# Kernel optimization log

Hardware: AMD Instinct MI355X
Metric: run time of the kernel (lower is better)

The kernel has to match this reference:

```python
import jax, jax.numpy as jnp
import numpy as np

B, XL, QL, VL, D = 8, 128, 16, 256, 256


def setup_inputs() -> dict:
    key = jax.random.key(0)
    ks = jax.random.split(key, 10)
    q = jax.random.normal(ks[0], (B, XL, QL, D), dtype=jnp.float32)
    k = jax.random.normal(ks[1], (B, XL, VL, D), dtype=jnp.float32)
    v = jax.random.normal(ks[2], (B, XL, VL, D), dtype=jnp.float32)
    # mask==True means position is masked out (filled with -10 before softmax)
    mask = jax.random.bernoulli(ks[3], 0.3, (B, XL, VL))
    s = 1.0 / np.sqrt(D)
    qw_w = jax.random.uniform(ks[4], (D, D), jnp.float32, -s, s)
    qw_b = jax.random.uniform(ks[5], (D,), jnp.float32, -s, s)
    kw_w = jax.random.uniform(ks[6], (D, D), jnp.float32, -s, s)
    kw_b = jax.random.uniform(ks[7], (D,), jnp.float32, -s, s)
    vw_w = jax.random.uniform(ks[8], (D, D), jnp.float32, -s, s)
    vw_b = jax.random.uniform(ks[9], (D,), jnp.float32, -s, s)
    return {"q": q, "k": k, "v": v, "mask": mask,
            "qw_w": qw_w, "qw_b": qw_b, "kw_w": kw_w, "kw_b": kw_b,
            "vw_w": vw_w, "vw_b": vw_b}


def reference(q, k, v, mask, qw_w, qw_b, kw_w, kw_b, vw_w, vw_b):
    # Linear projections (torch Linear: x @ W.T + b)
    qp = q @ qw_w.T + qw_b          # [b, x_l, q_l, d]
    kp = k @ kw_w.T + kw_b          # [b, x_l, v_l, d]
    vp = v @ vw_w.T + vw_b          # [b, x_l, v_l, d]
    # QK^T then max-pool over the q_l axis -> one score per value token
    scores = jnp.einsum('bxqd,bxvd->bxqv', qp, kp)   # [b, x_l, q_l, v_l]
    ta = jnp.max(scores, axis=-2)                    # [b, x_l, v_l]
    # L2-normalize over v_l (computed BEFORE masking, as in the original)
    ta = ta / jnp.linalg.norm(ta, axis=-1, keepdims=True)
    # rows where every position is masked (no words)
    nowords = jnp.sum(~mask, axis=-1) == 0           # [b, x_l]
    ta = jnp.where(mask, jnp.float32(-10.0), ta)
    attn = jax.nn.softmax(ta, axis=-1)               # [b, x_l, v_l]
    attn = jnp.where(nowords[..., None], jnp.float32(0.0), attn)
    out = jnp.einsum('bxv,bxvd->bxd', attn, vp)      # [b, x_l, d]
    return out[:, :, None, :]                        # [b, x_l, 1, d]
```

## Files before the change

kernel.cpp:

```cpp
#include <hip/hip_runtime.h>
#include <hip/hip_bf16.h>

#define NPAIR 1024
#define DD    256
#define QL    16
#define VL    256
#define KSTR  264

#define WS_MB   1024
#define WS_U    2048
#define WS_MT   4096
#define WS_VWT  135168

typedef __bf16 bf16x8 __attribute__((ext_vector_type(8)));
typedef __bf16 bf16x4 __attribute__((ext_vector_type(4)));
typedef float  f32x4  __attribute__((ext_vector_type(4)));

__global__ __launch_bounds__(256) void sa_precompute(const float* __restrict__ qw,
                                                     const float* __restrict__ qb,
                                                     const float* __restrict__ kw,
                                                     const float* __restrict__ kb,
                                                     const float* __restrict__ vww,
                                                     const unsigned int* __restrict__ maskw,
                                                     char* __restrict__ ws) {
    int c = blockIdx.x, e = threadIdx.x;
    float acc = 0.f;
    #pragma unroll 16
    for (int d = 0; d < 256; ++d) acc += qw[d*256 + e] * kw[d*256 + c];
    ((__bf16*)(ws + WS_MT))[c*256 + e] = (__bf16)acc;

    ((float*)(ws + WS_VWT))[(c >> 2)*1024 + e*4 + (c & 3)] = vww[e*256 + c];

    if (c == 0) {
        float a2 = 0.f;
        #pragma unroll 16
        for (int d = 0; d < 256; ++d) a2 += qb[d] * kw[d*256 + e];
        ((float*)(ws + WS_MB))[e] = a2;
    } else if (c == 1) {
        float a2 = 0.f;
        #pragma unroll 16
        for (int d = 0; d < 256; ++d) a2 += qw[d*256 + e] * kb[d];
        ((float*)(ws + WS_U))[e] = a2;
    } else if (c == 2 && e == 0) {
        float a2 = 0.f;
        #pragma unroll 16
        for (int d = 0; d < 256; ++d) a2 += qb[d] * kb[d];
        ((float*)(ws + 4))[0] = a2;
    } else if (c == 3) {
        __shared__ int f;
        if (e == 0) f = 0;
        __syncthreads();
        if (maskw[e] & ~1u) atomicOr(&f, 1);
        __syncthreads();
        if (e == 0) *(int*)ws = f;
    }
}

__device__ __forceinline__ float blockReduceSum(float v, float* red, int tid) {
    __syncthreads();
    #pragma unroll
    for (int off = 32; off >= 1; off >>= 1) v += __shfl_xor(v, off);
    if ((tid & 63) == 0) red[tid >> 6] = v;
    __syncthreads();
    return (red[0] + red[1]) + (red[2] + red[3]);
}

__global__ __launch_bounds__(256) void sa_fused(const float* __restrict__ qg,
                                                const float* __restrict__ kg,
                                                const float* __restrict__ vg,
                                                const void*  __restrict__ maskp,
                                                const float* __restrict__ vwb,
                                                const char*  __restrict__ ws,
                                                float* __restrict__ outp) {
    const int p    = blockIdx.x;
    const int tid  = threadIdx.x;
    const int lane = tid & 63;
    const int w    = tid >> 6;
    const int col  = lane & 15;
    const int quad = lane >> 4;

    const int    flag = *(const int*)ws;
    const float  s0   = *(const float*)(ws + 4);
    const float* mb   = (const float*)(ws + WS_MB);
    const float* u    = (const float*)(ws + WS_U);
    const __bf16* MT  = (const __bf16*)(ws + WS_MT);

    const float* Q = qg + (size_t)p * (QL * DD);
    const float* K = kg + (size_t)p * (VL * DD);
    const float* V = vg + (size_t)p * (VL * DD);

    __shared__ __align__(16) __bf16 q_lds[16 * KSTR];
    __shared__ __align__(16) __bf16 qk_lds[16 * KSTR];
    __shared__ __align__(16) float part[256];
    __shared__ float sbias_lds[16];
    __shared__ __align__(16) float ta_lds[256];
    __shared__ __align__(16) float attn_lds[256];
    __shared__ __align__(16) float wpart[4][256];
    __shared__ __align__(16) float w_lds[256];
    __shared__ float red[4];

    {
        const float4* Q4 = (const float4*)Q;
        #pragma unroll
        for (int it = 0; it < 4; ++it) {
            int idx = tid + it * 256;
            float4 v4 = Q4[idx];
            int f = idx * 4; int i = f >> 8; int e = f & 255;
            bf16x4 t; t[0] = (__bf16)v4.x; t[1] = (__bf16)v4.y;
                      t[2] = (__bf16)v4.z; t[3] = (__bf16)v4.w;
            *(bf16x4*)(&q_lds[i * KSTR + e]) = t;
        }
    }
    {
        int i = tid >> 4, seg = tid & 15;
        float s = 0.f;
        const float* qrow = Q + i * DD + seg * 16;
        const float* useg = u + seg * 16;
        #pragma unroll
        for (int e = 0; e < 16; ++e) s += qrow[e] * useg[e];
        part[i * 16 + seg] = s;
    }
    __syncthreads();
    if (tid < 16) {
        float s = s0;
        #pragma unroll
        for (int seg = 0; seg < 16; ++seg) s += part[tid * 16 + seg];
        sbias_lds[tid] = s;
    }

    {
        #pragma unroll
        for (int t = 0; t < 4; ++t) {
            int cc = (w * 4 + t) * 16 + col;
            float mbv = mb[cc];
            f32x4 acc; acc[0] = mbv; acc[1] = mbv; acc[2] = mbv; acc[3] = mbv;
            const __bf16* arow = &q_lds[col * KSTR + quad * 8];
            const __bf16* brow = &MT[(size_t)cc * 256 + quad * 8];
            #pragma unroll
            for (int k0 = 0; k0 < 256; k0 += 32) {
                bf16x8 a = *(const bf16x8*)(arow + k0);
                bf16x8 b = *(const bf16x8*)(brow + k0);
                acc = __builtin_amdgcn_mfma_f32_16x16x32_bf16(a, b, acc, 0, 0, 0);
            }
            #pragma unroll
            for (int r = 0; r < 4; ++r)
                qk_lds[(quad * 4 + r) * KSTR + cc] = (__bf16)acc[r];
        }
    }
    __syncthreads();

    {
        bf16x8 afrag[8];
        #pragma unroll
        for (int s = 0; s < 8; ++s)
            afrag[s] = *(const bf16x8*)(&qk_lds[col * KSTR + quad * 8 + s * 32]);

        #pragma unroll 1
        for (int vt = 0; vt < 4; ++vt) {
            int vrow = vt * 64 + w * 16 + col;
            const float* Krow = K + (size_t)vrow * DD + quad * 8;
            float4 b0[8], b1[8];
            #pragma unroll
            for (int s = 0; s < 8; ++s) {
                b0[s] = *(const float4*)(Krow + s * 32);
                b1[s] = *(const float4*)(Krow + s * 32 + 4);
            }
            f32x4 acc;
            #pragma unroll
            for (int r = 0; r < 4; ++r) acc[r] = sbias_lds[quad * 4 + r];
            #pragma unroll
            for (int s = 0; s < 8; ++s) {
                bf16x8 b;
                b[0] = (__bf16)b0[s].x; b[1] = (__bf16)b0[s].y;
                b[2] = (__bf16)b0[s].z; b[3] = (__bf16)b0[s].w;
                b[4] = (__bf16)b1[s].x; b[5] = (__bf16)b1[s].y;
                b[6] = (__bf16)b1[s].z; b[7] = (__bf16)b1[s].w;
                acc = __builtin_amdgcn_mfma_f32_16x16x32_bf16(afrag[s], b, acc, 0, 0, 0);
            }
            float m4 = fmaxf(fmaxf(acc[0], acc[1]), fmaxf(acc[2], acc[3]));
            m4 = fmaxf(m4, __shfl_xor(m4, 16));
            m4 = fmaxf(m4, __shfl_xor(m4, 32));
            if (quad == 0) ta_lds[vrow] = m4;
        }
    }
    __syncthreads();

    float S;
    {
        float myv = ta_lds[tid];
        float ssq = blockReduceSum(myv * myv, red, tid);
        float rn  = 1.0f / sqrtf(ssq);
        bool masked;
        if (flag) masked = ((const unsigned char*)maskp)[(size_t)p * 256 + tid] != 0;
        else      masked = ((const int*)maskp)[(size_t)p * 256 + tid] != 0;
        float cnt = blockReduceSum(masked ? 0.f : 1.f, red, tid);
        float val = masked ? -10.f : (myv * rn);
        float ex  = expf(val);
        float se  = blockReduceSum(ex, red, tid);
        S = (cnt == 0.f) ? 0.f : 1.f;
        attn_lds[tid] = (cnt == 0.f) ? 0.f : (ex / se);
    }
    __syncthreads();

    {
        const f32x4* V4 = (const f32x4*)V;
        f32x4 wa; wa[0] = 0.f; wa[1] = 0.f; wa[2] = 0.f; wa[3] = 0.f;
        #pragma unroll 4
        for (int j = 0; j < 64; ++j) {
            int row = (j << 2) | w;
            float a = attn_lds[row];
            f32x4 r4 = V4[row * 64 + lane];
            wa += a * r4;
        }
        *(f32x4*)&wpart[w][lane * 4] = wa;
    }
    __syncthreads();
    w_lds[tid] = (wpart[0][tid] + wpart[1][tid]) + (wpart[2][tid] + wpart[3][tid]);
    __syncthreads();

    {
        const f32x4* T4 = (const f32x4*)(ws + WS_VWT);
        f32x4 acc4; acc4[0] = 0.f; acc4[1] = 0.f; acc4[2] = 0.f; acc4[3] = 0.f;
        #pragma unroll 8
        for (int cq = 0; cq < 64; ++cq) {
            f32x4 m4 = T4[cq * 256 + tid];
            f32x4 wv = *(const f32x4*)&w_lds[cq * 4];
            acc4 += m4 * wv;
        }
        float accO = vwb[tid] * S + (acc4[0] + acc4[1]) + (acc4[2] + acc4[3]);
        outp[(size_t)p * 256 + tid] = accO;
    }
}

extern "C" void kernel_launch(void* const* d_in, const int* in_sizes, int n_in,
                              void* d_out, int out_size, void* d_ws, size_t ws_size,
                              hipStream_t stream) {
    const float* q    = (const float*)d_in[0];
    const float* k    = (const float*)d_in[1];
    const float* v    = (const float*)d_in[2];
    const void*  mask = d_in[3];
    const float* qw_w = (const float*)d_in[4];
    const float* qw_b = (const float*)d_in[5];
    const float* kw_w = (const float*)d_in[6];
    const float* kw_b = (const float*)d_in[7];
    const float* vw_w = (const float*)d_in[8];
    const float* vw_b = (const float*)d_in[9];

    char* ws = (char*)d_ws;

    hipLaunchKernelGGL(sa_precompute, dim3(256), dim3(256), 0, stream,
                       qw_w, qw_b, kw_w, kw_b, vw_w, (const unsigned int*)mask, ws);
    hipLaunchKernelGGL(sa_fused, dim3(NPAIR), dim3(256), 0, stream,
                       q, k, v, mask, vw_b, (const char*)ws, (float*)d_out);
}
```

Baseline: 555.0 us.

## Software-pipeline K, V and weight loads with register double-buffering

Issues the first K tile loads before the Q/QK phase, then prefetches the next K tile while computing MFMAs on the current one. V rows are preloaded into two register buffers before the softmax reductions, and the transposed weight matrix is prefetched before the barrier, with ping-pong reloads inside the loops. It also merges two block reductions into one and adds an occupancy hint to launch bounds. The aim is to hide global-memory latency in this memory-bound per-pair kernel, at the cost of much higher register pressure that could cause spills or lower occupancy.

```diff
diff --git a/kernel.cpp b/kernel.cpp
--- a/kernel.cpp
+++ b/kernel.cpp
@@ -65,13 +65,25 @@
     return (red[0] + red[1]) + (red[2] + red[3]);
 }
 
-__global__ __launch_bounds__(256) void sa_fused(const float* __restrict__ qg,
-                                                const float* __restrict__ kg,
-                                                const float* __restrict__ vg,
-                                                const void*  __restrict__ maskp,
-                                                const float* __restrict__ vwb,
-                                                const char*  __restrict__ ws,
-                                                float* __restrict__ outp) {
+__device__ __forceinline__ float2 blockReduceSum2(float a, float b, float* red, int tid) {
+    __syncthreads();
+    #pragma unroll
+    for (int off = 32; off >= 1; off >>= 1) { a += __shfl_xor(a, off); b += __shfl_xor(b, off); }
+    if ((tid & 63) == 0) { red[tid >> 6] = a; red[4 + (tid >> 6)] = b; }
+    __syncthreads();
+    float2 r;
+    r.x = (red[0] + red[1]) + (red[2] + red[3]);
+    r.y = (red[4] + red[5]) + (red[6] + red[7]);
+    return r;
+}
+
+__global__ __launch_bounds__(256, 4) void sa_fused(const float* __restrict__ qg,
+                                                   const float* __restrict__ kg,
+                                                   const float* __restrict__ vg,
+                                                   const void*  __restrict__ maskp,
+                                                   const float* __restrict__ vwb,
+                                                   const char*  __restrict__ ws,
+                                                   float* __restrict__ outp) {
     const int p    = blockIdx.x;
     const int tid  = threadIdx.x;
     const int lane = tid & 63;
@@ -97,7 +109,17 @@
     __shared__ __align__(16) float attn_lds[256];
     __shared__ __align__(16) float wpart[4][256];
     __shared__ __align__(16) float w_lds[256];
-    __shared__ float red[4];
+    __shared__ float red[8];
+
+    float4 F0[8], F1[8];
+    {
+        const float* Krow0 = K + (size_t)(w * 16 + col) * DD + quad * 8;
+        #pragma unroll
+        for (int s = 0; s < 8; ++s) {
+            F0[s] = *(const float4*)(Krow0 + s * 32);
+            F1[s] = *(const float4*)(Krow0 + s * 32 + 4);
+        }
+    }
 
     {
         const float4* Q4 = (const float4*)Q;
@@ -154,29 +176,28 @@
         #pragma unroll
         for (int s = 0; s < 8; ++s)
             afrag[s] = *(const bf16x8*)(&qk_lds[col * KSTR + quad * 8 + s * 32]);
+        float sb[4];
+        #pragma unroll
+        for (int r = 0; r < 4; ++r) sb[r] = sbias_lds[quad * 4 + r];
 
         #pragma unroll 1
         for (int vt = 0; vt < 4; ++vt) {
-            int vrow = vt * 64 + w * 16 + col;
-            const float* Krow = K + (size_t)vrow * DD + quad * 8;
-            float4 b0[8], b1[8];
-            #pragma unroll
-            for (int s = 0; s < 8; ++s) {
-                b0[s] = *(const float4*)(Krow + s * 32);
-                b1[s] = *(const float4*)(Krow + s * 32 + 4);
-            }
-            f32x4 acc;
-            #pragma unroll
-            for (int r = 0; r < 4; ++r) acc[r] = sbias_lds[quad * 4 + r];
+            const float* KrowN = K + (size_t)((vt + 1) * 64 + w * 16 + col) * DD + quad * 8;
+            f32x4 acc; acc[0] = sb[0]; acc[1] = sb[1]; acc[2] = sb[2]; acc[3] = sb[3];
             #pragma unroll
             for (int s = 0; s < 8; ++s) {
                 bf16x8 b;
-                b[0] = (__bf16)b0[s].x; b[1] = (__bf16)b0[s].y;
-                b[2] = (__bf16)b0[s].z; b[3] = (__bf16)b0[s].w;
-                b[4] = (__bf16)b1[s].x; b[5] = (__bf16)b1[s].y;
-                b[6] = (__bf16)b1[s].z; b[7] = (__bf16)b1[s].w;
+                b[0] = (__bf16)F0[s].x; b[1] = (__bf16)F0[s].y;
+                b[2] = (__bf16)F0[s].z; b[3] = (__bf16)F0[s].w;
+                b[4] = (__bf16)F1[s].x; b[5] = (__bf16)F1[s].y;
+                b[6] = (__bf16)F1[s].z; b[7] = (__bf16)F1[s].w;
+                if (vt < 3) {
+                    F0[s] = *(const float4*)(KrowN + s * 32);
+                    F1[s] = *(const float4*)(KrowN + s * 32 + 4);
+                }
                 acc = __builtin_amdgcn_mfma_f32_16x16x32_bf16(afrag[s], b, acc, 0, 0, 0);
             }
+            int vrow = vt * 64 + w * 16 + col;
             float m4 = fmaxf(fmaxf(acc[0], acc[1]), fmaxf(acc[2], acc[3]));
             m4 = fmaxf(m4, __shfl_xor(m4, 16));
             m4 = fmaxf(m4, __shfl_xor(m4, 32));
@@ -185,15 +206,22 @@
     }
     __syncthreads();
 
+    const f32x4* V4 = (const f32x4*)V;
+    f32x4 vbA[8], vbB[8];
+    #pragma unroll
+    for (int j = 0; j < 8; ++j) vbA[j] = V4[((j << 2) | w) * 64 + lane];
+    #pragma unroll
+    for (int j = 0; j < 8; ++j) vbB[j] = V4[(((8 + j) << 2) | w) * 64 + lane];
+
     float S;
     {
         float myv = ta_lds[tid];
-        float ssq = blockReduceSum(myv * myv, red, tid);
-        float rn  = 1.0f / sqrtf(ssq);
         bool masked;
         if (flag) masked = ((const unsigned char*)maskp)[(size_t)p * 256 + tid] != 0;
         else      masked = ((const int*)maskp)[(size_t)p * 256 + tid] != 0;
-        float cnt = blockReduceSum(masked ? 0.f : 1.f, red, tid);
+        float2 sc = blockReduceSum2(myv * myv, masked ? 0.f : 1.f, red, tid);
+        float rn  = 1.0f / sqrtf(sc.x);
+        float cnt = sc.y;
         float val = masked ? -10.f : (myv * rn);
         float ex  = expf(val);
         float se  = blockReduceSum(ex, red, tid);
@@ -203,29 +231,54 @@
     __syncthreads();
 
     {
-        const f32x4* V4 = (const f32x4*)V;
         f32x4 wa; wa[0] = 0.f; wa[1] = 0.f; wa[2] = 0.f; wa[3] = 0.f;
-        #pragma unroll 4
-        for (int j = 0; j < 64; ++j) {
-            int row = (j << 2) | w;
-            float a = attn_lds[row];
-            f32x4 r4 = V4[row * 64 + lane];
-            wa += a * r4;
+        #pragma unroll 1
+        for (int g = 0; g < 8; g += 2) {
+            #pragma unroll
+            for (int j = 0; j < 8; ++j) {
+                int j2 = g * 8 + j;
+                wa += attn_lds[(j2 << 2) | w] * vbA[j];
+                if (g + 2 < 8) vbA[j] = V4[((((g + 2) * 8 + j) << 2) | w) * 64 + lane];
+            }
+            #pragma unroll
+            for (int j = 0; j < 8; ++j) {
+                int j2 = (g + 1) * 8 + j;
+                wa += attn_lds[(j2 << 2) | w] * vbB[j];
+                if (g + 3 < 8) vbB[j] = V4[((((g + 3) * 8 + j) << 2) | w) * 64 + lane];
+            }
         }
         *(f32x4*)&wpart[w][lane * 4] = wa;
     }
+
+    const f32x4* T4 = (const f32x4*)(ws + WS_VWT);
+    f32x4 mA[8], mB[8];
+    #pragma unroll
+    for (int r = 0; r < 8; ++r) mA[r] = T4[r * 256 + tid];
+    #pragma unroll
+    for (int r = 0; r < 8; ++r) mB[r] = T4[(8 + r) * 256 + tid];
+
     __syncthreads();
     w_lds[tid] = (wpart[0][tid] + wpart[1][tid]) + (wpart[2][tid] + wpart[3][tid]);
     __syncthreads();
 
     {
-        const f32x4* T4 = (const f32x4*)(ws + WS_VWT);
         f32x4 acc4; acc4[0] = 0.f; acc4[1] = 0.f; acc4[2] = 0.f; acc4[3] = 0.f;
-        #pragma unroll 8
-        for (int cq = 0; cq < 64; ++cq) {
-            f32x4 m4 = T4[cq * 256 + tid];
-            f32x4 wv = *(const f32x4*)&w_lds[cq * 4];
-            acc4 += m4 * wv;
+        #pragma unroll 1
+        for (int g = 0; g < 8; g += 2) {
+            #pragma unroll
+            for (int r = 0; r < 8; ++r) {
+                int cq = g * 8 + r;
+                f32x4 wv = *(const f32x4*)&w_lds[cq * 4];
+                acc4 += mA[r] * wv;
+                if (g + 2 < 8) mA[r] = T4[((g + 2) * 8 + r) * 256 + tid];
+            }
+            #pragma unroll
+            for (int r = 0; r < 8; ++r) {
+                int cq = (g + 1) * 8 + r;
+                f32x4 wv = *(const f32x4*)&w_lds[cq * 4];
+                acc4 += mB[r] * wv;
+                if (g + 3 < 8) mB[r] = T4[((g + 3) * 8 + r) * 256 + tid];
+            }
         }
         float accO = vwb[tid] * S + (acc4[0] + acc4[1]) + (acc4[2] + acc4[3]);
         outp[(size_t)p * 256 + tid] = accO;
```

After: 723.2 us. 30.3% more time.
